# Optimization experiments

Measured on AMD Instinct MI355X. Metric: run time of the kernel, lower is better.

The kernel has to match this reference:

```python
import jax, jax.numpy as jnp
import numpy as np

NUM_USERS = 100000
NUM_ITEMS = 200000
D = 128          # embedding_dim
K = 4            # num interest heads
B = 4096
H = 256          # history length
H1, H2 = 512, 256  # hidden_units


def setup_inputs() -> dict:
    key = jax.random.key(0)
    ks = jax.random.split(key, 10)
    inp = {
        "user_ids": jax.random.randint(ks[0], (B,), 0, NUM_USERS),
        "candidate_items": jax.random.randint(ks[1], (B,), 0, NUM_ITEMS),
        "history_items": jax.random.randint(ks[2], (B, H), 0, NUM_ITEMS),
        "item_table": jax.random.normal(ks[3], (NUM_ITEMS, D), dtype=jnp.float32) * 0.05,
        "Wp": jax.random.normal(ks[4], (D, K), dtype=jnp.float32) * (1.0 / np.sqrt(D)),
        "W1": jax.random.normal(ks[5], (2 * D, H1), dtype=jnp.float32) * (1.0 / np.sqrt(2 * D)),
        "b1": jnp.zeros((H1,), dtype=jnp.float32),
        "W2": jax.random.normal(ks[6], (H1, H2), dtype=jnp.float32) * (1.0 / np.sqrt(H1)),
        "b2": jnp.zeros((H2,), dtype=jnp.float32),
        "W3": jax.random.normal(ks[7], (H2, 1), dtype=jnp.float32) * (1.0 / np.sqrt(H2)),
        "b3": jnp.zeros((1,), dtype=jnp.float32),
    }
    return inp


def reference(user_ids, candidate_items, history_items, item_table, Wp,
              W1, b1, W2, b2, W3, b3):
    # user_ids is unused by the original forward (user_emb never applied)
    item_vecs = item_table[history_items]          # (B, H, D)
    cand_vec = item_table[candidate_items]         # (B, D)

    # per-interest attention scores, softmax over history axis
    scores = jnp.einsum('bhd,dk->bhk', item_vecs, Wp)   # (B, H, K)
    scores = jax.nn.softmax(scores, axis=1)

    # softmax-weighted pooling -> K interest vectors per user
    interest_vectors = jnp.einsum('bhk,bhd->bkd', scores, item_vecs)  # (B, K, D)

    # similarity to candidate, pick best interest (data-dependent gather)
    sim_scores = jnp.einsum('bkd,bd->bk', interest_vectors, cand_vec)  # (B, K)
    best_idx = jnp.argmax(sim_scores, axis=-1)                          # (B,)
    selected = jnp.take_along_axis(
        interest_vectors, best_idx[:, None, None], axis=1)[:, 0, :]    # (B, D)

    # MLP tail: [2D -> 512] ReLU [512 -> 256] ReLU [256 -> 1], sigmoid
    x = jnp.concatenate([selected, cand_vec], axis=-1)  # (B, 2D)
    x = jax.nn.relu(x @ W1 + b1)
    x = jax.nn.relu(x @ W2 + b2)
    out = (x @ W3 + b3)[:, 0]                            # (B,)
    return jax.nn.sigmoid(out)
```

## Files before the change

kernel.cpp:

```cpp
#include <hip/hip_runtime.h>
#include <hip/hip_bf16.h>
#include <math.h>

#define B_SZ   4096
#define H_LEN  256
#define D_DIM  128
#define K_HEADS 4
#define H1_DIM 512
#define H2_DIM 256

#define CH     64
#define NCH    4
#define TPAD   132

typedef __attribute__((ext_vector_type(8))) short bf16x8;
typedef __attribute__((ext_vector_type(4))) float f32x4;

__global__ __launch_bounds__(256, 4) void interest_kernel(
    const int*   __restrict__ cand_ids,
    const int*   __restrict__ hist,
    const float* __restrict__ table,
    const float* __restrict__ Wp,
    __hip_bfloat16* __restrict__ Xbf)
{
    __shared__ float tile[CH * TPAD];
    __shared__ float wpt[K_HEADS * D_DIM];
    __shared__ float exps4[CH * 4];
    __shared__ float candv[D_DIM];
    __shared__ int   rowids[H_LEN];
    __shared__ float lsumW[16];
    __shared__ float simred[4][K_HEADS];
    __shared__ int   bestk;

    const int b    = blockIdx.x;
    const int t    = threadIdx.x;
    const int lane = t & 63, w = t >> 6;
    const int r    = t >> 2, q = t & 3;
    const int d    = t & 127, half = t >> 7;

    if (t < D_DIM) {
        float4 w4 = ((const float4*)Wp)[t];
        wpt[0 * D_DIM + t] = w4.x;
        wpt[1 * D_DIM + t] = w4.y;
        wpt[2 * D_DIM + t] = w4.z;
        wpt[3 * D_DIM + t] = w4.w;
    }
    const int cand = cand_ids[b];
    if (t >= 128 && t < 160) {
        int c = t - 128;
        ((float4*)candv)[c] = ((const float4*)(table + (long long)cand * D_DIM))[c];
    }
    rowids[t] = hist[(long long)b * H_LEN + t];

    float a0 = 0.f, a1 = 0.f, a2 = 0.f, a3 = 0.f;
    float l0 = 0.f, l1 = 0.f, l2 = 0.f, l3 = 0.f;

    for (int c = 0; c < NCH; ++c) {
        __syncthreads();

        const int   row = rowids[(c << 6) + r];
        const float* rp = table + (long long)row * D_DIM + (q << 2);
        float4 v0 = *(const float4*)(rp + 0 * 16);
        float4 v1 = *(const float4*)(rp + 1 * 16);
        float4 v2 = *(const float4*)(rp + 2 * 16);
        float4 v3 = *(const float4*)(rp + 3 * 16);
        float4 v4 = *(const float4*)(rp + 4 * 16);
        float4 v5 = *(const float4*)(rp + 5 * 16);
        float4 v6 = *(const float4*)(rp + 6 * 16);
        float4 v7 = *(const float4*)(rp + 7 * 16);

        float s0 = 0.f, s1 = 0.f, s2 = 0.f, s3 = 0.f;
        float4 va;
        #define DO_J(J, VV)                                                     \
        {   va = VV;                                                            \
            const int cb = (q << 2) + (J << 4);                                 \
            float4 w0 = *(const float4*)(wpt + 0 * D_DIM + cb);                 \
            float4 w1 = *(const float4*)(wpt + 1 * D_DIM + cb);                 \
            float4 w2 = *(const float4*)(wpt + 2 * D_DIM + cb);                 \
            float4 w3 = *(const float4*)(wpt + 3 * D_DIM + cb);                 \
            s0 += va.x * w0.x + va.y * w0.y + va.z * w0.z + va.w * w0.w;        \
            s1 += va.x * w1.x + va.y * w1.y + va.z * w1.z + va.w * w1.w;        \
            s2 += va.x * w2.x + va.y * w2.y + va.z * w2.z + va.w * w2.w;        \
            s3 += va.x * w3.x + va.y * w3.y + va.z * w3.z + va.w * w3.w;        \
            *(float4*)(tile + r * TPAD + cb) = va;                              \
        }
        DO_J(0, v0) DO_J(1, v1) DO_J(2, v2) DO_J(3, v3)
        DO_J(4, v4) DO_J(5, v5) DO_J(6, v6) DO_J(7, v7)
        #undef DO_J

        s0 += __shfl_xor(s0, 1); s0 += __shfl_xor(s0, 2);
        s1 += __shfl_xor(s1, 1); s1 += __shfl_xor(s1, 2);
        s2 += __shfl_xor(s2, 1); s2 += __shfl_xor(s2, 2);
        s3 += __shfl_xor(s3, 1); s3 += __shfl_xor(s3, 2);

        float e0 = expf(s0), e1 = expf(s1), e2 = expf(s2), e3 = expf(s3);
        if (q == 0) ((float4*)exps4)[r] = make_float4(e0, e1, e2, e3);

        float t0 = e0, t1 = e1, t2 = e2, t3 = e3;
        #pragma unroll
        for (int off = 4; off <= 32; off <<= 1) {
            t0 += __shfl_xor(t0, off);
            t1 += __shfl_xor(t1, off);
            t2 += __shfl_xor(t2, off);
            t3 += __shfl_xor(t3, off);
        }
        l0 += t0; l1 += t1; l2 += t2; l3 += t3;

        __syncthreads();

        #pragma unroll 8
        for (int i = 0; i < 32; ++i) {
            int hl = (half << 5) + i;
            float4 e4 = ((const float4*)exps4)[hl];
            float  vv = tile[hl * TPAD + d];
            a0 += e4.x * vv; a1 += e4.y * vv; a2 += e4.z * vv; a3 += e4.w * vv;
        }
    }

    __syncthreads();
    float* partBp = tile;
    float* ivbufp = tile + 512;

    if (half == 1) ((float4*)partBp)[d] = make_float4(a0, a1, a2, a3);
    if (lane == 0) ((float4*)lsumW)[w]  = make_float4(l0, l1, l2, l3);
    __syncthreads();

    float s0 = 0.f, s1 = 0.f, s2 = 0.f, s3 = 0.f;
    if (half == 0) {
        float4 pb = ((const float4*)partBp)[d];
        float4 L0 = ((const float4*)lsumW)[0];
        float4 L1 = ((const float4*)lsumW)[1];
        float4 L2 = ((const float4*)lsumW)[2];
        float4 L3 = ((const float4*)lsumW)[3];
        float i0 = 1.f / (L0.x + L1.x + L2.x + L3.x);
        float i1 = 1.f / (L0.y + L1.y + L2.y + L3.y);
        float i2 = 1.f / (L0.z + L1.z + L2.z + L3.z);
        float i3 = 1.f / (L0.w + L1.w + L2.w + L3.w);
        a0 = (a0 + pb.x) * i0;
        a1 = (a1 + pb.y) * i1;
        a2 = (a2 + pb.z) * i2;
        a3 = (a3 + pb.w) * i3;
        ((float4*)ivbufp)[d] = make_float4(a0, a1, a2, a3);
        float cd = candv[d];
        s0 = a0 * cd; s1 = a1 * cd; s2 = a2 * cd; s3 = a3 * cd;
    }
    #pragma unroll
    for (int off = 32; off >= 1; off >>= 1) {
        s0 += __shfl_xor(s0, off);
        s1 += __shfl_xor(s1, off);
        s2 += __shfl_xor(s2, off);
        s3 += __shfl_xor(s3, off);
    }
    if (lane == 0) {
        simred[w][0] = s0; simred[w][1] = s1;
        simred[w][2] = s2; simred[w][3] = s3;
    }
    __syncthreads();

    if (t == 0) {
        float sim[4];
        #pragma unroll
        for (int k = 0; k < 4; ++k)
            sim[k] = simred[0][k] + simred[1][k] + simred[2][k] + simred[3][k];
        int best = 0;
        #pragma unroll
        for (int k = 1; k < 4; ++k) if (sim[k] > sim[best]) best = k;
        bestk = best;
    }
    __syncthreads();

    __hip_bfloat16* xrow = Xbf + (long long)b * (2 * D_DIM);
    if (t < 128) xrow[t] = __float2bfloat16(ivbufp[t * 4 + bestk]);
    else         xrow[t] = __float2bfloat16(candv[t - 128]);
}

__global__ __launch_bounds__(256) void convert_weights(
    const float* __restrict__ W1, const float* __restrict__ W2,
    __hip_bfloat16* __restrict__ W1t, __hip_bfloat16* __restrict__ W2t)
{
    int idx = blockIdx.x * 256 + threadIdx.x;
    if (idx < 2 * D_DIM * H1_DIM) {
        int n = idx >> 8, k = idx & 255;
        W1t[idx] = __float2bfloat16(W1[k * H1_DIM + n]);
    } else {
        int j = idx - 2 * D_DIM * H1_DIM;
        int n = j >> 9, k = j & 511;
        W2t[j] = __float2bfloat16(W2[k * H2_DIM + n]);
    }
}

template<int N, int K, bool OUT_BF16>
__global__ __launch_bounds__(256) void mfma_mlp(
    const __hip_bfloat16* __restrict__ A,
    const __hip_bfloat16* __restrict__ Bt,
    const float* __restrict__ bias,
    void* __restrict__ Cout)
{
    const int t    = threadIdx.x;
    const int wave = t >> 6, lane = t & 63;
    const int lm   = lane & 15, quad = lane >> 4;
    const int n0   = blockIdx.x * 16;
    const int m0   = blockIdx.y * 64 + wave * 16;

    const __hip_bfloat16* Ap = A  + (long long)(m0 + lm) * K + quad * 8;
    const __hip_bfloat16* Bp = Bt + (long long)(n0 + lm) * K + quad * 8;

    f32x4 acc = {0.f, 0.f, 0.f, 0.f};
    for (int kc = 0; kc < K; kc += 256) {
        bf16x8 af[8], bfr[8];
        #pragma unroll
        for (int it = 0; it < 8; ++it) {
            af[it]  = *(const bf16x8*)(Ap + kc + it * 32);
            bfr[it] = *(const bf16x8*)(Bp + kc + it * 32);
        }
        #pragma unroll
        for (int it = 0; it < 8; ++it)
            acc = __builtin_amdgcn_mfma_f32_16x16x32_bf16(af[it], bfr[it], acc, 0, 0, 0);
    }

    const int n  = n0 + lm;
    const float bv = bias[n];
    #pragma unroll
    for (int i = 0; i < 4; ++i) {
        int m = m0 + quad * 4 + i;
        float v = fmaxf(acc[i] + bv, 0.f);
        if (OUT_BF16)
            ((__hip_bfloat16*)Cout)[(long long)m * N + n] = __float2bfloat16(v);
        else
            ((float*)Cout)[(long long)m * N + n] = v;
    }
}

__global__ __launch_bounds__(256) void head_kernel(
    const float* __restrict__ H2buf,
    const float* __restrict__ W3,
    const float* __restrict__ b3,
    float*       __restrict__ out)
{
    const int b = blockIdx.x * 256 + threadIdx.x;
    const float4* hp = (const float4*)(H2buf + (long long)b * H2_DIM);
    const float4* wp = (const float4*)W3;
    float acc = 0.f;
    #pragma unroll 8
    for (int i = 0; i < H2_DIM / 4; ++i) {
        float4 h = hp[i], wv = wp[i];
        acc += h.x * wv.x + h.y * wv.y + h.z * wv.z + h.w * wv.w;
    }
    float z = acc + b3[0];
    out[b] = 1.f / (1.f + expf(-z));
}

extern "C" void kernel_launch(void* const* d_in, const int* in_sizes, int n_in,
                              void* d_out, int out_size, void* d_ws, size_t ws_size,
                              hipStream_t stream) {
    const int*   cand  = (const int*)  d_in[1];
    const int*   hist  = (const int*)  d_in[2];
    const float* table = (const float*)d_in[3];
    const float* Wp    = (const float*)d_in[4];
    const float* W1    = (const float*)d_in[5];
    const float* b1    = (const float*)d_in[6];
    const float* W2    = (const float*)d_in[7];
    const float* b2    = (const float*)d_in[8];
    const float* W3    = (const float*)d_in[9];
    const float* b3    = (const float*)d_in[10];
    float* out = (float*)d_out;

    char* p = (char*)d_ws;
    __hip_bfloat16* Xbf  = (__hip_bfloat16*)p;                  p += (size_t)B_SZ * 2 * D_DIM * 2;
    __hip_bfloat16* Hc1  = (__hip_bfloat16*)p;                  p += (size_t)B_SZ * H1_DIM * 2;
    float*          Hc2  = (float*)p;                           p += (size_t)B_SZ * H2_DIM * 4;
    __hip_bfloat16* W1t  = (__hip_bfloat16*)p;                  p += (size_t)H1_DIM * 2 * D_DIM * 2;
    __hip_bfloat16* W2t  = (__hip_bfloat16*)p;

    convert_weights<<<(2 * D_DIM * H1_DIM + H1_DIM * H2_DIM) / 256, 256, 0, stream>>>(
        W1, W2, W1t, W2t);
    interest_kernel<<<B_SZ, 256, 0, stream>>>(cand, hist, table, Wp, Xbf);
    mfma_mlp<H1_DIM, 2 * D_DIM, true><<<dim3(H1_DIM / 16, B_SZ / 64), 256, 0, stream>>>(
        Xbf, W1t, b1, Hc1);
    mfma_mlp<H2_DIM, H1_DIM, false><<<dim3(H2_DIM / 16, B_SZ / 64), 256, 0, stream>>>(
        Hc1, W2t, b2, Hc2);
    head_kernel<<<B_SZ / 256, 256, 0, stream>>>(Hc2, W3, b3, out);
}
```

Baseline: 275.2 us.

## Fuse MLP layers and head into one kernel, prefetch history chunks, tile weight transpose

The two MFMA GEMM kernels and the sigmoid head are merged into one kernel that processes 16 rows per block and keeps the hidden activations in shared memory. This removes the global round-trips for the H1 and H2 intermediates and two launches. The interest kernel now loads the next history chunk into registers while the current one is processed, to hide gather latency, at the cost of higher register pressure. The weight transpose-and-convert kernel uses a shared-memory tile so its reads and writes are both coalesced.

```diff
diff --git a/kernel.cpp b/kernel.cpp
--- a/kernel.cpp
+++ b/kernel.cpp
@@ -52,22 +52,40 @@
     }
     rowids[t] = hist[(long long)b * H_LEN + t];
 
+    __syncthreads();
+
     float a0 = 0.f, a1 = 0.f, a2 = 0.f, a3 = 0.f;
     float l0 = 0.f, l1 = 0.f, l2 = 0.f, l3 = 0.f;
 
+    float4 v0, v1, v2, v3, v4, v5, v6, v7;
+    {
+        const int row = rowids[r];
+        const float* rp = table + (long long)row * D_DIM + (q << 2);
+        v0 = *(const float4*)(rp + 0 * 16);
+        v1 = *(const float4*)(rp + 1 * 16);
+        v2 = *(const float4*)(rp + 2 * 16);
+        v3 = *(const float4*)(rp + 3 * 16);
+        v4 = *(const float4*)(rp + 4 * 16);
+        v5 = *(const float4*)(rp + 5 * 16);
+        v6 = *(const float4*)(rp + 6 * 16);
+        v7 = *(const float4*)(rp + 7 * 16);
+    }
+
+    #pragma unroll
     for (int c = 0; c < NCH; ++c) {
-        __syncthreads();
-
-        const int   row = rowids[(c << 6) + r];
-        const float* rp = table + (long long)row * D_DIM + (q << 2);
-        float4 v0 = *(const float4*)(rp + 0 * 16);
-        float4 v1 = *(const float4*)(rp + 1 * 16);
-        float4 v2 = *(const float4*)(rp + 2 * 16);
-        float4 v3 = *(const float4*)(rp + 3 * 16);
-        float4 v4 = *(const float4*)(rp + 4 * 16);
-        float4 v5 = *(const float4*)(rp + 5 * 16);
-        float4 v6 = *(const float4*)(rp + 6 * 16);
-        float4 v7 = *(const float4*)(rp + 7 * 16);
+        float4 u0, u1, u2, u3, u4, u5, u6, u7;
+        if (c + 1 < NCH) {
+            const int row = rowids[((c + 1) << 6) + r];
+            const float* rp = table + (long long)row * D_DIM + (q << 2);
+            u0 = *(const float4*)(rp + 0 * 16);
+            u1 = *(const float4*)(rp + 1 * 16);
+            u2 = *(const float4*)(rp + 2 * 16);
+            u3 = *(const float4*)(rp + 3 * 16);
+            u4 = *(const float4*)(rp + 4 * 16);
+            u5 = *(const float4*)(rp + 5 * 16);
+            u6 = *(const float4*)(rp + 6 * 16);
+            u7 = *(const float4*)(rp + 7 * 16);
+        }
 
         float s0 = 0.f, s1 = 0.f, s2 = 0.f, s3 = 0.f;
         float4 va;
@@ -82,7 +100,7 @@
             s1 += va.x * w1.x + va.y * w1.y + va.z * w1.z + va.w * w1.w;        \
             s2 += va.x * w2.x + va.y * w2.y + va.z * w2.z + va.w * w2.w;        \
             s3 += va.x * w3.x + va.y * w3.y + va.z * w3.z + va.w * w3.w;        \
-            *(float4*)(tile + r * TPAD + cb) = va;                              \
+            *(float4*)(tile + (t >> 2) * TPAD + cb) = va;                       \
         }
         DO_J(0, v0) DO_J(1, v1) DO_J(2, v2) DO_J(3, v3)
         DO_J(4, v4) DO_J(5, v5) DO_J(6, v6) DO_J(7, v7)
@@ -115,9 +133,13 @@
             float  vv = tile[hl * TPAD + d];
             a0 += e4.x * vv; a1 += e4.y * vv; a2 += e4.z * vv; a3 += e4.w * vv;
         }
-    }
-
-    __syncthreads();
+
+        __syncthreads();
+
+        v0 = u0; v1 = u1; v2 = u2; v3 = u3;
+        v4 = u4; v5 = u5; v6 = u6; v7 = u7;
+    }
+
     float* partBp = tile;
     float* ivbufp = tile + 512;
 
@@ -178,76 +200,96 @@
     const float* __restrict__ W1, const float* __restrict__ W2,
     __hip_bfloat16* __restrict__ W1t, __hip_bfloat16* __restrict__ W2t)
 {
-    int idx = blockIdx.x * 256 + threadIdx.x;
-    if (idx < 2 * D_DIM * H1_DIM) {
-        int n = idx >> 8, k = idx & 255;
-        W1t[idx] = __float2bfloat16(W1[k * H1_DIM + n]);
-    } else {
-        int j = idx - 2 * D_DIM * H1_DIM;
-        int n = j >> 9, k = j & 511;
-        W2t[j] = __float2bfloat16(W2[k * H2_DIM + n]);
-    }
+    __shared__ float tl[32][33];
+    int bid = blockIdx.x;
+    const float* W; __hip_bfloat16* Wt; int K, N;
+    if (bid < 128) { W = W1; Wt = W1t; K = 2 * D_DIM; N = H1_DIM; }
+    else           { W = W2; Wt = W2t; K = H1_DIM;    N = H2_DIM; bid -= 128; }
+    const int ntn = N >> 5;
+    const int k0 = (bid / ntn) << 5, n0 = (bid % ntn) << 5;
+    const int tx = threadIdx.x & 31, ty = threadIdx.x >> 5;
+    #pragma unroll
+    for (int j = 0; j < 4; ++j)
+        tl[ty + 8 * j][tx] = W[(long long)(k0 + ty + 8 * j) * N + n0 + tx];
+    __syncthreads();
+    #pragma unroll
+    for (int j = 0; j < 4; ++j)
+        Wt[(long long)(n0 + ty + 8 * j) * K + k0 + tx] =
+            __float2bfloat16(tl[tx][ty + 8 * j]);
 }
 
-template<int N, int K, bool OUT_BF16>
-__global__ __launch_bounds__(256) void mfma_mlp(
-    const __hip_bfloat16* __restrict__ A,
-    const __hip_bfloat16* __restrict__ Bt,
-    const float* __restrict__ bias,
-    void* __restrict__ Cout)
-{
-    const int t    = threadIdx.x;
-    const int wave = t >> 6, lane = t & 63;
-    const int lm   = lane & 15, quad = lane >> 4;
-    const int n0   = blockIdx.x * 16;
-    const int m0   = blockIdx.y * 64 + wave * 16;
-
-    const __hip_bfloat16* Ap = A  + (long long)(m0 + lm) * K + quad * 8;
-    const __hip_bfloat16* Bp = Bt + (long long)(n0 + lm) * K + quad * 8;
-
-    f32x4 acc = {0.f, 0.f, 0.f, 0.f};
-    for (int kc = 0; kc < K; kc += 256) {
-        bf16x8 af[8], bfr[8];
-        #pragma unroll
-        for (int it = 0; it < 8; ++it) {
-            af[it]  = *(const bf16x8*)(Ap + kc + it * 32);
-            bfr[it] = *(const bf16x8*)(Bp + kc + it * 32);
-        }
-        #pragma unroll
-        for (int it = 0; it < 8; ++it)
-            acc = __builtin_amdgcn_mfma_f32_16x16x32_bf16(af[it], bfr[it], acc, 0, 0, 0);
-    }
-
-    const int n  = n0 + lm;
-    const float bv = bias[n];
-    #pragma unroll
-    for (int i = 0; i < 4; ++i) {
-        int m = m0 + quad * 4 + i;
-        float v = fmaxf(acc[i] + bv, 0.f);
-        if (OUT_BF16)
-            ((__hip_bfloat16*)Cout)[(long long)m * N + n] = __float2bfloat16(v);
-        else
-            ((float*)Cout)[(long long)m * N + n] = v;
-    }
-}
-
-__global__ __launch_bounds__(256) void head_kernel(
-    const float* __restrict__ H2buf,
+__global__ __launch_bounds__(512) void mlp_fused(
+    const __hip_bfloat16* __restrict__ X,
+    const __hip_bfloat16* __restrict__ W1t,
+    const float* __restrict__ b1,
+    const __hip_bfloat16* __restrict__ W2t,
+    const float* __restrict__ b2,
     const float* __restrict__ W3,
     const float* __restrict__ b3,
     float*       __restrict__ out)
 {
-    const int b = blockIdx.x * 256 + threadIdx.x;
-    const float4* hp = (const float4*)(H2buf + (long long)b * H2_DIM);
-    const float4* wp = (const float4*)W3;
-    float acc = 0.f;
-    #pragma unroll 8
-    for (int i = 0; i < H2_DIM / 4; ++i) {
-        float4 h = hp[i], wv = wp[i];
-        acc += h.x * wv.x + h.y * wv.y + h.z * wv.z + h.w * wv.w;
-    }
-    float z = acc + b3[0];
-    out[b] = 1.f / (1.f + expf(-z));
+    __shared__ __hip_bfloat16 h1[16][H1_DIM + 8];
+    __shared__ float          h2[16][H2_DIM + 4];
+
+    const int t    = threadIdx.x;
+    const int wave = t >> 6, lane = t & 63;
+    const int lm   = lane & 15, quad = lane >> 4;
+    const int m0   = blockIdx.x * 16;
+
+    const __hip_bfloat16* Ap = X + (long long)(m0 + lm) * (2 * D_DIM) + quad * 8;
+    bf16x8 af[8];
+    #pragma unroll
+    for (int it = 0; it < 8; ++it) af[it] = *(const bf16x8*)(Ap + it * 32);
+
+    #pragma unroll
+    for (int tn = 0; tn < 4; ++tn) {
+        const int n0 = (wave * 4 + tn) * 16;
+        const __hip_bfloat16* Bp = W1t + (long long)(n0 + lm) * (2 * D_DIM) + quad * 8;
+        f32x4 acc = {0.f, 0.f, 0.f, 0.f};
+        #pragma unroll
+        for (int it = 0; it < 8; ++it) {
+            bf16x8 bfr = *(const bf16x8*)(Bp + it * 32);
+            acc = __builtin_amdgcn_mfma_f32_16x16x32_bf16(af[it], bfr, acc, 0, 0, 0);
+        }
+        const float bv = b1[n0 + lm];
+        #pragma unroll
+        for (int i = 0; i < 4; ++i)
+            h1[quad * 4 + i][n0 + lm] = __float2bfloat16(fmaxf(acc[i] + bv, 0.f));
+    }
+    __syncthreads();
+
+    bf16x8 a2[16];
+    #pragma unroll
+    for (int it = 0; it < 16; ++it)
+        a2[it] = *(const bf16x8*)(&h1[lm][quad * 8 + it * 32]);
+
+    #pragma unroll
+    for (int tn = 0; tn < 2; ++tn) {
+        const int n0 = (wave * 2 + tn) * 16;
+        const __hip_bfloat16* Bp = W2t + (long long)(n0 + lm) * H1_DIM + quad * 8;
+        f32x4 acc = {0.f, 0.f, 0.f, 0.f};
+        #pragma unroll
+        for (int it = 0; it < 16; ++it) {
+            bf16x8 bfr = *(const bf16x8*)(Bp + it * 32);
+            acc = __builtin_amdgcn_mfma_f32_16x16x32_bf16(a2[it], bfr, acc, 0, 0, 0);
+        }
+        const float bv = b2[n0 + lm];
+        #pragma unroll
+        for (int i = 0; i < 4; ++i)
+            h2[quad * 4 + i][n0 + lm] = fmaxf(acc[i] + bv, 0.f);
+    }
+    __syncthreads();
+
+    {
+        const int row = t >> 5, c = (t & 31) * 8;
+        float s = 0.f;
+        #pragma unroll
+        for (int j = 0; j < 8; ++j) s += h2[row][c + j] * W3[c + j];
+        #pragma unroll
+        for (int off = 1; off <= 16; off <<= 1) s += __shfl_xor(s, off);
+        if ((lane & 31) == 0)
+            out[m0 + row] = 1.f / (1.f + expf(-(s + b3[0])));
+    }
 }
 
 extern "C" void kernel_launch(void* const* d_in, const int* in_sizes, int n_in,
@@ -266,18 +308,11 @@
     float* out = (float*)d_out;
 
     char* p = (char*)d_ws;
-    __hip_bfloat16* Xbf  = (__hip_bfloat16*)p;                  p += (size_t)B_SZ * 2 * D_DIM * 2;
-    __hip_bfloat16* Hc1  = (__hip_bfloat16*)p;                  p += (size_t)B_SZ * H1_DIM * 2;
-    float*          Hc2  = (float*)p;                           p += (size_t)B_SZ * H2_DIM * 4;
-    __hip_bfloat16* W1t  = (__hip_bfloat16*)p;                  p += (size_t)H1_DIM * 2 * D_DIM * 2;
-    __hip_bfloat16* W2t  = (__hip_bfloat16*)p;
-
-    convert_weights<<<(2 * D_DIM * H1_DIM + H1_DIM * H2_DIM) / 256, 256, 0, stream>>>(
-        W1, W2, W1t, W2t);
+    __hip_bfloat16* Xbf = (__hip_bfloat16*)p;  p += (size_t)B_SZ * 2 * D_DIM * 2;
+    __hip_bfloat16* W1t = (__hip_bfloat16*)p;  p += (size_t)H1_DIM * 2 * D_DIM * 2;
+    __hip_bfloat16* W2t = (__hip_bfloat16*)p;
+
+    convert_weights<<<256, 256, 0, stream>>>(W1, W2, W1t, W2t);
     interest_kernel<<<B_SZ, 256, 0, stream>>>(cand, hist, table, Wp, Xbf);
-    mfma_mlp<H1_DIM, 2 * D_DIM, true><<<dim3(H1_DIM / 16, B_SZ / 64), 256, 0, stream>>>(
-        Xbf, W1t, b1, Hc1);
-    mfma_mlp<H2_DIM, H1_DIM, false><<<dim3(H2_DIM / 16, B_SZ / 64), 256, 0, stream>>>(
-        Hc1, W2t, b2, Hc2);
-    head_kernel<<<B_SZ / 256, 256, 0, stream>>>(Hc2, W3, b3, out);
+    mlp_fused<<<B_SZ / 16, 512, 0, stream>>>(Xbf, W1t, b1, W2t, b2, W3, b3, out);
 }
```

Result: faster. 259.5 us (-5.7%).
